# Kernel tuning notes

Hardware: AMD Instinct MI355X
Metric: run time of the kernel (lower is better)

The kernel has to match this reference:

```python
import jax, jax.numpy as jnp
import numpy as np

B = 524288   # Monte-Carlo sample batch
C = 64       # C1 hidden width
D = 4        # D1 hidden layers
L = 4        # positional encoding frequencies
CIN = (2 * L + 1) * 2 + 2  # cond (18) + z (2) = 20
EPS = 1e-12


def posenc(x):
    # x: (B,2) -> (B, 2*(2L+1)) : identity + sin/cos at 2^i frequencies
    feats = [x]
    for i in range(L):
        f = (2.0 ** i) * x
        feats.append(jnp.sin(f))
        feats.append(jnp.cos(f))
    return jnp.concatenate(feats, -1)


def mlp(x, W_in, b_in, W_hid, b_hid, W_out, b_out):
    h = jax.nn.silu(x @ W_in + b_in)
    for i in range(W_hid.shape[0]):  # small fixed layer count
        h = jax.nn.silu(h @ W_hid[i] + b_hid[i])
    return h @ W_out + b_out


def forward_wi(cond, z, W_in, b_in, W_hid, b_hid, W_out, b_out):
    Tz = mlp(jnp.concatenate([cond, z], -1), W_in, b_in, W_hid, b_hid, W_out, b_out)
    wi3 = jnp.concatenate([Tz[..., :2], jax.nn.softplus(Tz[..., 2:])], -1)
    norm = jnp.maximum(jnp.linalg.norm(wi3, axis=-1, keepdims=True), EPS)
    wi3 = wi3 / norm  # F.normalize
    return wi3[..., :2]


def setup_inputs() -> dict:
    key = jax.random.key(0)
    ks = jax.random.split(key, 8)
    wo = jax.random.uniform(ks[0], (B, 2), dtype=jnp.float32)
    z = jax.random.normal(ks[1], (B, 2), dtype=jnp.float32)
    W_in = jax.random.normal(ks[2], (CIN, C), dtype=jnp.float32) / np.sqrt(CIN)
    b_in = jnp.zeros((C,), jnp.float32)
    W_hid = jax.random.normal(ks[3], (D - 1, C, C), dtype=jnp.float32) / np.sqrt(C)
    b_hid = jnp.zeros((D - 1, C), jnp.float32)
    W_out = jax.random.normal(ks[4], (C, 3), dtype=jnp.float32) / np.sqrt(C)
    b_out = jnp.zeros((3,), jnp.float32)
    return dict(wo=wo, z=z, W_in=W_in, b_in=b_in, W_hid=W_hid, b_hid=b_hid,
                W_out=W_out, b_out=b_out)


def reference(wo, z, W_in, b_in, W_hid, b_hid, W_out, b_out):
    cond = posenc(wo)  # (B,18)
    f = lambda zz: forward_wi(cond, zz, W_in, b_in, W_hid, b_hid, W_out, b_out)
    # 2x2 Jacobian via two batched JVPs (columns of J)
    t0 = jnp.broadcast_to(jnp.array([1.0, 0.0], jnp.float32), z.shape)
    t1 = jnp.broadcast_to(jnp.array([0.0, 1.0], jnp.float32), z.shape)
    wi, d0 = jax.jvp(f, (z,), (t0,))  # d0 = dwi/dz0, (B,2)
    _, d1 = jax.jvp(f, (z,), (t1,))  # d1 = dwi/dz1, (B,2)
    detJ = d0[..., 0] * d1[..., 1] - d1[..., 0] * d0[..., 1]
    # pack (wi, detJ) as (B,3) for a single-array output
    return jnp.concatenate([wi, detJ[..., None]], -1)
```

## Files before the change

kernel.cpp:

```cpp
#include <hip/hip_runtime.h>
#include <math.h>


#define SAMP 64
#define NTHR 192
#define C 64

__device__ __forceinline__ float frcp(float x) { return __builtin_amdgcn_rcpf(x); }
__device__ __forceinline__ float fsig(float a) { return frcp(1.f + __expf(-a)); }

__global__ __launch_bounds__(NTHR, 3) void neu_kernel(
    const float* __restrict__ wo, const float* __restrict__ z,
    const float* __restrict__ W_in, const float* __restrict__ b_in,
    const float* __restrict__ W_hid, const float* __restrict__ b_hid,
    const float* __restrict__ W_out, const float* __restrict__ b_out,
    float* __restrict__ out)
{
    __shared__ float sh_sp[2][C*SAMP];

    const int tid  = threadIdx.x;
    const int samp = tid & 63;
    const int wave = __builtin_amdgcn_readfirstlane(tid >> 6);
    const int gs   = blockIdx.x * SAMP + samp;

    float s[C];
    float u[C];

    {
        float x[20];
        const float2 wv = *reinterpret_cast<const float2*>(wo + gs*2);
        x[0] = wv.x; x[1] = wv.y;
        float f0 = wv.x, f1 = wv.y;
        #pragma unroll
        for (int i = 0; i < 4; ++i) {
            x[2+4*i+0] = __sinf(f0);
            x[2+4*i+1] = __sinf(f1);
            x[2+4*i+2] = __cosf(f0);
            x[2+4*i+3] = __cosf(f1);
            f0 += f0; f1 += f1;
        }
        const float2 zv = *reinterpret_cast<const float2*>(z + gs*2);
        x[18] = zv.x;
        x[19] = zv.y;

        #pragma unroll
        for (int c = 0; c < 2; ++c) {
            const int c0 = c * 32;
            {
                const float* wr = W_in + 0*C + c0;
                #pragma unroll
                for (int j = 0; j < 32; ++j) u[c0+j] = fmaf(x[0], wr[j], b_in[c0+j]);
            }
            #pragma unroll
            for (int k = 1; k < 20; ++k) {
                const float xk = x[k];
                const float* wr = W_in + k*C + c0;
                #pragma unroll
                for (int j = 0; j < 32; ++j) u[c0+j] = fmaf(xk, wr[j], u[c0+j]);
            }
        }
        if (wave == 0) {
            #pragma unroll
            for (int j = 0; j < 64; ++j) {
                float a = u[j];
                s[j] = a * fsig(a);
            }
        } else {
            const float* wr = W_in + (17 + wave)*C;
            #pragma unroll
            for (int j = 0; j < 64; ++j) {
                float a  = u[j];
                float sg = fsig(a);
                float sp = sg * (1.f + a * (1.f - sg));
                s[j] = sp * wr[j];
            }
        }
    }

    for (int l = 0; l < 3; ++l) {
        const float* Wl = W_hid + l*C*C;
        #pragma unroll
        for (int c = 0; c < 2; ++c) {
            const int c0 = c * 32;
            {
                const float s0 = s[0];
                const float* wr = Wl + c0;
                #pragma unroll
                for (int j = 0; j < 32; ++j) u[c0+j] = s0 * wr[j];
            }
            #pragma unroll
            for (int k = 1; k < C; ++k) {
                const float sk = s[k];
                const float* wr = Wl + k*C + c0;
                #pragma unroll
                for (int j = 0; j < 32; ++j) u[c0+j] = fmaf(sk, wr[j], u[c0+j]);
            }
        }
        float* buf = sh_sp[l & 1];
        if (wave == 0) {
            const float* bh = b_hid + l*C;
            #pragma unroll
            for (int j = 0; j < 64; ++j) {
                float a  = u[j] + bh[j];
                float sg = fsig(a);
                s[j] = a * sg;
                buf[j*SAMP + samp] = sg * (1.f + a * (1.f - sg));
            }
        }
        __syncthreads();
        if (wave != 0) {
            #pragma unroll
            for (int j = 0; j < 64; ++j) {
                s[j] = buf[j*SAMP + samp] * u[j];
            }
        }
    }

    {
        float o0, o1, o2;
        if (wave == 0) { o0 = b_out[0]; o1 = b_out[1]; o2 = b_out[2]; }
        else           { o0 = 0.f;      o1 = 0.f;      o2 = 0.f;      }
        #pragma unroll
        for (int k = 0; k < C; ++k) {
            o0 = fmaf(s[k], W_out[k*3+0], o0);
            o1 = fmaf(s[k], W_out[k*3+1], o1);
            o2 = fmaf(s[k], W_out[k*3+2], o2);
        }
        float* st = sh_sp[1];
        st[(wave*3+0)*SAMP + samp] = o0;
        st[(wave*3+1)*SAMP + samp] = o1;
        st[(wave*3+2)*SAMP + samp] = o2;
    }
    __syncthreads();
    if (wave == 0) {
        const float* st = sh_sp[1];
        float T0 = st[0*SAMP+samp], T1 = st[1*SAMP+samp], T2 = st[2*SAMP+samp];
        float a0 = st[3*SAMP+samp], a1 = st[4*SAMP+samp], a2 = st[5*SAMP+samp];
        float c0 = st[6*SAMP+samp], c1 = st[7*SAMP+samp], c2 = st[8*SAMP+samp];
        float sg2 = 1.f / (1.f + expf(-T2));
        float u2  = fmaxf(T2, 0.f) + log1pf(expf(-fabsf(T2)));
        float u0 = T0, u1 = T1;
        float n2  = u0*u0 + u1*u1 + u2*u2;
        float n   = fmaxf(sqrtf(n2), 1e-12f);
        float inv = 1.f / n;
        float da2 = sg2 * a2, dc2 = sg2 * c2;
        float ka  = (u0*a0 + u1*a1 + u2*da2) / n2;
        float kc  = (u0*c0 + u1*c1 + u2*dc2) / n2;
        float d0x = (a0 - u0*ka) * inv;
        float d0y = (a1 - u1*ka) * inv;
        float d1x = (c0 - u0*kc) * inv;
        float d1y = (c1 - u1*kc) * inv;
        float detJ = d0x*d1y - d1x*d0y;
        out[gs*3+0] = u0 * inv;
        out[gs*3+1] = u1 * inv;
        out[gs*3+2] = detJ;
    }
}

extern "C" void kernel_launch(void* const* d_in, const int* in_sizes, int n_in,
                              void* d_out, int out_size, void* d_ws, size_t ws_size,
                              hipStream_t stream) {
    const float* wo    = (const float*)d_in[0];
    const float* zz    = (const float*)d_in[1];
    const float* W_in  = (const float*)d_in[2];
    const float* b_in  = (const float*)d_in[3];
    const float* W_hid = (const float*)d_in[4];
    const float* b_hid = (const float*)d_in[5];
    const float* W_out = (const float*)d_in[6];
    const float* b_out = (const float*)d_in[7];
    float* o = (float*)d_out;

    const int B = in_sizes[0] / 2;
    const int nblk = B / SAMP;
    neu_kernel<<<nblk, NTHR, 0, stream>>>(wo, zz, W_in, b_in, W_hid, b_hid,
                                          W_out, b_out, o);
}
```

Measured before the change: 628.7 us.

## Spill part of per-sample activations to LDS to raise occupancy

Keeps only 48 of the 64 activation/tangent values in registers and parks the remaining 16 per wave in LDS, while raising the launch-bounds occupancy hint from 3 to 4 blocks per CU. Wave 0 now publishes pre-activations rather than silu derivatives, so the tangent waves compute the sigmoid derivative themselves. The output-column loop is also no longer split into two 32-wide halves. The aim is lower VGPR pressure and more resident waves to hide latency. The cost is extra LDS traffic, redundant sigmoid work in the tangent waves, and a second __syncthreads per layer.

```diff
diff --git a/kernel.cpp b/kernel.cpp
--- a/kernel.cpp
+++ b/kernel.cpp
@@ -5,25 +5,33 @@
 #define SAMP 64
 #define NTHR 192
 #define C 64
+#define JR 48
+#define JS (C - JR)
 
 __device__ __forceinline__ float frcp(float x) { return __builtin_amdgcn_rcpf(x); }
 __device__ __forceinline__ float fsig(float a) { return frcp(1.f + __expf(-a)); }
-
-__global__ __launch_bounds__(NTHR, 3) void neu_kernel(
+__device__ __forceinline__ float fsp(float a, float sg) {
+    return sg * (1.f + a * (1.f - sg));
+}
+
+__global__ __launch_bounds__(NTHR, 4) void neu_kernel(
     const float* __restrict__ wo, const float* __restrict__ z,
     const float* __restrict__ W_in, const float* __restrict__ b_in,
     const float* __restrict__ W_hid, const float* __restrict__ b_hid,
     const float* __restrict__ W_out, const float* __restrict__ b_out,
     float* __restrict__ out)
 {
-    __shared__ float sh_sp[2][C*SAMP];
+    __shared__ float sh_a[C*SAMP];
+    __shared__ float sh_sx[3][JS*SAMP];
 
     const int tid  = threadIdx.x;
     const int samp = tid & 63;
     const int wave = __builtin_amdgcn_readfirstlane(tid >> 6);
     const int gs   = blockIdx.x * SAMP + samp;
 
-    float s[C];
+    float* sx = sh_sx[wave];
+
+    float s[JR];
     float u[C];
 
     {
@@ -43,77 +51,91 @@
         x[18] = zv.x;
         x[19] = zv.y;
 
-        #pragma unroll
-        for (int c = 0; c < 2; ++c) {
-            const int c0 = c * 32;
-            {
-                const float* wr = W_in + 0*C + c0;
-                #pragma unroll
-                for (int j = 0; j < 32; ++j) u[c0+j] = fmaf(x[0], wr[j], b_in[c0+j]);
-            }
-            #pragma unroll
-            for (int k = 1; k < 20; ++k) {
-                const float xk = x[k];
-                const float* wr = W_in + k*C + c0;
-                #pragma unroll
-                for (int j = 0; j < 32; ++j) u[c0+j] = fmaf(xk, wr[j], u[c0+j]);
-            }
+        {
+            const float* wr = W_in;
+            #pragma unroll
+            for (int j = 0; j < C; ++j) u[j] = fmaf(x[0], wr[j], b_in[j]);
+        }
+        #pragma unroll
+        for (int k = 1; k < 20; ++k) {
+            const float xk = x[k];
+            const float* wr = W_in + k*C;
+            #pragma unroll
+            for (int j = 0; j < C; ++j) u[j] = fmaf(xk, wr[j], u[j]);
         }
         if (wave == 0) {
             #pragma unroll
-            for (int j = 0; j < 64; ++j) {
-                float a = u[j];
-                s[j] = a * fsig(a);
-            }
+            for (int j = 0; j < JR; ++j) { float a = u[j]; s[j] = a * fsig(a); }
+            #pragma unroll
+            for (int j = JR; j < C; ++j) { float a = u[j]; sx[(j-JR)*SAMP+samp] = a * fsig(a); }
         } else {
             const float* wr = W_in + (17 + wave)*C;
             #pragma unroll
-            for (int j = 0; j < 64; ++j) {
-                float a  = u[j];
-                float sg = fsig(a);
-                float sp = sg * (1.f + a * (1.f - sg));
-                s[j] = sp * wr[j];
+            for (int j = 0; j < JR; ++j) {
+                float a = u[j], sg = fsig(a);
+                s[j] = fsp(a, sg) * wr[j];
+            }
+            #pragma unroll
+            for (int j = JR; j < C; ++j) {
+                float a = u[j], sg = fsig(a);
+                sx[(j-JR)*SAMP+samp] = fsp(a, sg) * wr[j];
             }
         }
     }
 
     for (int l = 0; l < 3; ++l) {
         const float* Wl = W_hid + l*C*C;
-        #pragma unroll
-        for (int c = 0; c < 2; ++c) {
-            const int c0 = c * 32;
-            {
-                const float s0 = s[0];
-                const float* wr = Wl + c0;
+        {
+            const float m0 = s[0];
+            const float* wr = Wl;
+            #pragma unroll
+            for (int j = 0; j < C; ++j) u[j] = m0 * wr[j];
+        }
+        #pragma unroll
+        for (int k = 1; k < JR; ++k) {
+            const float m = s[k];
+            const float* wr = Wl + k*C;
+            #pragma unroll
+            for (int j = 0; j < C; ++j) u[j] = fmaf(m, wr[j], u[j]);
+        }
+        {
+            float st[JS];
+            #pragma unroll
+            for (int i = 0; i < JS; ++i) st[i] = sx[i*SAMP + samp];
+            #pragma unroll
+            for (int k = JR; k < C; ++k) {
+                const float m = st[k-JR];
+                const float* wr = Wl + k*C;
                 #pragma unroll
-                for (int j = 0; j < 32; ++j) u[c0+j] = s0 * wr[j];
-            }
-            #pragma unroll
-            for (int k = 1; k < C; ++k) {
-                const float sk = s[k];
-                const float* wr = Wl + k*C + c0;
-                #pragma unroll
-                for (int j = 0; j < 32; ++j) u[c0+j] = fmaf(sk, wr[j], u[c0+j]);
-            }
-        }
-        float* buf = sh_sp[l & 1];
+                for (int j = 0; j < C; ++j) u[j] = fmaf(m, wr[j], u[j]);
+            }
+        }
         if (wave == 0) {
             const float* bh = b_hid + l*C;
             #pragma unroll
-            for (int j = 0; j < 64; ++j) {
-                float a  = u[j] + bh[j];
-                float sg = fsig(a);
-                s[j] = a * sg;
-                buf[j*SAMP + samp] = sg * (1.f + a * (1.f - sg));
-            }
+            for (int j = 0; j < C; ++j) u[j] += bh[j];
+            #pragma unroll
+            for (int j = 0; j < C; ++j) sh_a[j*SAMP + samp] = u[j];
         }
         __syncthreads();
-        if (wave != 0) {
-            #pragma unroll
-            for (int j = 0; j < 64; ++j) {
-                s[j] = buf[j*SAMP + samp] * u[j];
-            }
-        }
+        if (wave == 0) {
+            #pragma unroll
+            for (int j = 0; j < JR; ++j) { float a = u[j]; s[j] = a * fsig(a); }
+            #pragma unroll
+            for (int j = JR; j < C; ++j) { float a = u[j]; sx[(j-JR)*SAMP+samp] = a * fsig(a); }
+        } else {
+            #pragma unroll
+            for (int j = 0; j < JR; ++j) {
+                float a = sh_a[j*SAMP + samp], sg = fsig(a);
+                s[j] = fsp(a, sg) * u[j];
+            }
+            #pragma unroll
+            for (int j = JR; j < C; ++j) {
+                float a = sh_a[j*SAMP + samp], sg = fsig(a);
+                sx[(j-JR)*SAMP+samp] = fsp(a, sg) * u[j];
+            }
+        }
+        __syncthreads();
     }
 
     {
@@ -121,22 +143,29 @@
         if (wave == 0) { o0 = b_out[0]; o1 = b_out[1]; o2 = b_out[2]; }
         else           { o0 = 0.f;      o1 = 0.f;      o2 = 0.f;      }
         #pragma unroll
-        for (int k = 0; k < C; ++k) {
+        for (int k = 0; k < JR; ++k) {
             o0 = fmaf(s[k], W_out[k*3+0], o0);
             o1 = fmaf(s[k], W_out[k*3+1], o1);
             o2 = fmaf(s[k], W_out[k*3+2], o2);
         }
-        float* st = sh_sp[1];
-        st[(wave*3+0)*SAMP + samp] = o0;
-        st[(wave*3+1)*SAMP + samp] = o1;
-        st[(wave*3+2)*SAMP + samp] = o2;
+        float st[JS];
+        #pragma unroll
+        for (int i = 0; i < JS; ++i) st[i] = sx[i*SAMP + samp];
+        #pragma unroll
+        for (int k = JR; k < C; ++k) {
+            o0 = fmaf(st[k-JR], W_out[k*3+0], o0);
+            o1 = fmaf(st[k-JR], W_out[k*3+1], o1);
+            o2 = fmaf(st[k-JR], W_out[k*3+2], o2);
+        }
+        sh_a[(wave*3+0)*SAMP + samp] = o0;
+        sh_a[(wave*3+1)*SAMP + samp] = o1;
+        sh_a[(wave*3+2)*SAMP + samp] = o2;
     }
     __syncthreads();
     if (wave == 0) {
-        const float* st = sh_sp[1];
-        float T0 = st[0*SAMP+samp], T1 = st[1*SAMP+samp], T2 = st[2*SAMP+samp];
-        float a0 = st[3*SAMP+samp], a1 = st[4*SAMP+samp], a2 = st[5*SAMP+samp];
-        float c0 = st[6*SAMP+samp], c1 = st[7*SAMP+samp], c2 = st[8*SAMP+samp];
+        float T0 = sh_a[0*SAMP+samp], T1 = sh_a[1*SAMP+samp], T2 = sh_a[2*SAMP+samp];
+        float a0 = sh_a[3*SAMP+samp], a1 = sh_a[4*SAMP+samp], a2 = sh_a[5*SAMP+samp];
+        float c0 = sh_a[6*SAMP+samp], c1 = sh_a[7*SAMP+samp], c2 = sh_a[8*SAMP+samp];
         float sg2 = 1.f / (1.f + expf(-T2));
         float u2  = fmaxf(T2, 0.f) + log1pf(expf(-fabsf(T2)));
         float u0 = T0, u1 = T1;
```

Result: no change. 623.3 us (-0.9%).
